# Performance work log

Measured on AMD Instinct MI355X. Metric: run time of the kernel, lower is better.

Reference implementation:

```python
import jax, jax.numpy as jnp
import numpy as np

ALPHA = 0.2  # LeakyReLU negative slope
NEG_INF = -9e15


def setup_inputs() -> dict:
    key = jax.random.key(0)
    k1, k2, k3, k4 = jax.random.split(key, 4)
    B, N, F_in, F_out = 8, 2048, 256, 128
    x = jax.random.normal(k1, (B, N, F_in), dtype=jnp.float32)
    adj = jax.random.randint(k2, (B, N, N), 0, 2, dtype=jnp.int32)
    # xavier-uniform-like init
    limW = float(np.sqrt(6.0 / (F_in + F_out)))
    W = jax.random.uniform(k3, (F_in, F_out), jnp.float32, -limW, limW)
    lima = float(np.sqrt(6.0 / (2 * F_out + 1)))
    a = jax.random.uniform(k4, (2 * F_out, 1), jnp.float32, -lima, lima)
    return {"x": x, "adj": adj, "W": W, "a": a}


def reference(x, adj, W, a):
    # x: [B, N, F_in], adj: [B, N, N], W: [F_in, F_out], a: [2*F_out, 1]
    F_out = W.shape[1]
    h = jnp.einsum('bnf,fo->bno', x, W)            # [B, N, F_out]
    a1 = a[:F_out, 0]                               # attends to source node i
    a2 = a[F_out:, 0]                               # attends to target node j
    f1 = h @ a1                                     # [B, N]
    f2 = h @ a2                                     # [B, N]
    # e[b,i,j] = leakyrelu(a1.h_i + a2.h_j) -- factored form of the concat trick
    e = jax.nn.leaky_relu(f1[:, :, None] + f2[:, None, :], negative_slope=ALPHA)
    attention = jnp.where(adj > 0, e, NEG_INF)
    attention = jax.nn.softmax(attention, axis=2)   # [B, N, N]
    # dropout is identity in eval mode
    h_prime = jnp.einsum('bij,bjo->bio', attention, h)  # [B, N, F_out]
    return jax.nn.elu(h_prime)                      # concat=True -> ELU
```

## Files before the change

### kernel.cpp

```cpp
#include <hip/hip_runtime.h>
#include <stdint.h>

#define BB   8
#define NN   2048
#define FIN  256
#define FOUT 128

using short8 = __attribute__((ext_vector_type(8))) short;
using f32x4  = __attribute__((ext_vector_type(4))) float;

__device__ __forceinline__ unsigned short rbf(float f) {
    return (unsigned short)((__float_as_uint(f) + 0x8000u) >> 16);
}

__device__ __forceinline__ void mfma_calib(int m, int quad, int* Mlab, int* Nlab) {
    short8 pa1, pb1, pa2, pb2;
    const short one = (short)0x3F80;
    const short mb  = (short)rbf((float)m);
#pragma unroll
    for (int j = 0; j < 8; ++j) { pa1[j] = 0; pa2[j] = 0; pb1[j] = mb; pb2[j] = one; }
    if (quad == 0) { pa1[0] = one; pa2[0] = mb; }
    f32x4 zz = {0.f, 0.f, 0.f, 0.f};
    f32x4 c1 = __builtin_amdgcn_mfma_f32_16x16x32_bf16(pa1, pb1, zz, 0, 0, 0);
    f32x4 c2 = __builtin_amdgcn_mfma_f32_16x16x32_bf16(pa2, pb2, zz, 0, 0, 0);
#pragma unroll
    for (int r = 0; r < 4; ++r) {
        Nlab[r] = ((int)c1[r]) & 15;
        Mlab[r] = ((int)c2[r]) & 15;
    }
}

__global__ __launch_bounds__(256) void gat_wt(const float* __restrict__ W,
                                              unsigned short* __restrict__ wt) {
    const int g  = blockIdx.x * 256 + threadIdx.x;
    const int k  = g >> 5;
    const int o4 = (g & 31) << 2;
    float4 wv = *(const float4*)(W + (k << 7) + o4);
    wt[((o4 + 0) << 8) + k] = rbf(wv.x);
    wt[((o4 + 1) << 8) + k] = rbf(wv.y);
    wt[((o4 + 2) << 8) + k] = rbf(wv.z);
    wt[((o4 + 3) << 8) + k] = rbf(wv.w);
}

__global__ __launch_bounds__(256) void gat_h3(
        const float* __restrict__ x, const unsigned short* __restrict__ wt,
        const float* __restrict__ a, unsigned short* __restrict__ ht,
        float* __restrict__ f1, float* __restrict__ f2) {
    __shared__ unsigned short xs[16][264];
    __shared__ float hs[16][132];
    const int bk   = blockIdx.x;
    const int R0   = bk << 4;
    const int b    = R0 >> 11;
    const int il0  = R0 & (NN - 1);
    const int tid  = threadIdx.x;
    const int w    = tid >> 6;
    const int lane = tid & 63;
    const int m    = lane & 15;
    const int quad = lane >> 4;

#pragma unroll
    for (int rr = 0; rr < 4; ++rr) {
        const int row = (w << 2) + rr;
        float4 xv = *(const float4*)(x + (size_t)(R0 + row) * FIN + (lane << 2));
        ushort4 c4;
        c4.x = rbf(xv.x); c4.y = rbf(xv.y); c4.z = rbf(xv.z); c4.w = rbf(xv.w);
        *(ushort4*)(&xs[row][lane << 2]) = c4;
    }
    int Mlab[4], Nlab[4];
    mfma_calib(m, quad, Mlab, Nlab);
    __syncthreads();

    f32x4 zz = {0.f, 0.f, 0.f, 0.f};
    f32x4 acc[2] = {zz, zz};
#pragma unroll
    for (int kc = 0; kc < 8; ++kc) {
        const int k0 = (kc << 5) + (quad << 3);
        short8 av = *(const short8*)(&xs[m][k0]);
#pragma unroll
        for (int t = 0; t < 2; ++t) {
            const int ot = (w << 1) + t;
            short8 bw = *(const short8*)(wt + (((ot << 4) + m) << 8) + k0);
            acc[t] = __builtin_amdgcn_mfma_f32_16x16x32_bf16(av, bw, acc[t], 0, 0, 0);
        }
    }
#pragma unroll
    for (int t = 0; t < 2; ++t)
#pragma unroll
        for (int r = 0; r < 4; ++r)
            hs[Mlab[r]][(((w << 1) + t) << 4) + Nlab[r]] = acc[t][r];
    __syncthreads();

    {
        const int i   = tid >> 4;
        const int seg = tid & 15;
        const int o0  = seg << 3;
        float s1 = 0.f, s2 = 0.f;
#pragma unroll
        for (int e = 0; e < 8; ++e) {
            float hv = hs[i][o0 + e];
            s1 = fmaf(hv, a[o0 + e], s1);
            s2 = fmaf(hv, a[FOUT + o0 + e], s2);
        }
        s1 += __shfl_xor(s1, 1); s1 += __shfl_xor(s1, 2);
        s1 += __shfl_xor(s1, 4); s1 += __shfl_xor(s1, 8);
        s2 += __shfl_xor(s2, 1); s2 += __shfl_xor(s2, 2);
        s2 += __shfl_xor(s2, 4); s2 += __shfl_xor(s2, 8);
        if (seg == 0) { f1[R0 + i] = s1; f2[R0 + i] = s2; }
    }
    {
        const int o  = tid >> 1;
        const int i8 = (tid & 1) << 3;
        short8 hv;
#pragma unroll
        for (int e = 0; e < 8; ++e) hv[e] = (short)rbf(hs[i8 + e][o]);
        *(short8*)(ht + ((size_t)((b << 7) + o) << 11) + il0 + i8) = hv;
    }
}

__global__ __launch_bounds__(256, 2) void gat_s4(
        const int* __restrict__ adj, const unsigned short* __restrict__ ht,
        const float* __restrict__ f1, const float* __restrict__ f2,
        float* __restrict__ out) {
    const int bk   = blockIdx.x;
    const int b    = bk & 7;
    const int i0   = (bk >> 3) << 5;
    const int tid  = threadIdx.x;
    const int w    = tid >> 6;
    const int lane = tid & 63;
    const int m    = lane & 15;
    const int quad = lane >> 4;

    __shared__ float accb[2][32][128];
    __shared__ float sbuf[4][2][16];

    int Mlab[4], Nlab[4];
    mfma_calib(m, quad, Mlab, Nlab);

    const int gi0 = (b << 11) + i0;
    const float f1a = f1[gi0 + m];
    const float f1b = f1[gi0 + 16 + m];
    const int* adjr0 = adj + ((size_t)(gi0 + m) << 11);
    const int* adjr1 = adj + ((size_t)(gi0 + 16 + m) << 11);
    const float* f2b = f2 + (b << 11);
    const unsigned short* htb = ht + ((size_t)b << 18);

    f32x4 zz = {0.f, 0.f, 0.f, 0.f};
    f32x4 acc1[8], acc2[8];
#pragma unroll
    for (int t = 0; t < 8; ++t) { acc1[t] = zz; acc2[t] = zz; }
    float s1 = 0.f, s2 = 0.f;

    const int jb = (w << 9) + (quad << 3);
#pragma unroll 2
    for (int c = 0; c < 16; ++c) {
        const int j0 = jb + (c << 5);
        short8 hf[8];
#pragma unroll
        for (int ot = 0; ot < 8; ++ot)
            hf[ot] = *(const short8*)(htb + ((size_t)((ot << 4) + m) << 11) + j0);

        int4   aA0 = *(const int4*)(adjr0 + j0);
        int4   aA1 = *(const int4*)(adjr0 + j0 + 4);
        int4   aB0 = *(const int4*)(adjr1 + j0);
        int4   aB1 = *(const int4*)(adjr1 + j0 + 4);
        float4 fa  = *(const float4*)(f2b + j0);
        float4 fb  = *(const float4*)(f2b + j0 + 4);
        float fm[8] = {fa.x, fa.y, fa.z, fa.w, fb.x, fb.y, fb.z, fb.w};

        float pA[8], pB[8];
        {
            int am[8] = {aA0.x, aA0.y, aA0.z, aA0.w, aA1.x, aA1.y, aA1.z, aA1.w};
#pragma unroll
            for (int u = 0; u < 8; ++u) {
                float e = f1a + fm[u];
                pA[u] = (am[u] > 0) ? __expf(fmaxf(e, 0.2f * e)) : 0.f;
            }
        }
        {
            int bm[8] = {aB0.x, aB0.y, aB0.z, aB0.w, aB1.x, aB1.y, aB1.z, aB1.w};
#pragma unroll
            for (int u = 0; u < 8; ++u) {
                float e = f1b + fm[u];
                pB[u] = (bm[u] > 0) ? __expf(fmaxf(e, 0.2f * e)) : 0.f;
            }
        }
        s1 += ((pA[0] + pA[1]) + (pA[2] + pA[3])) + ((pA[4] + pA[5]) + (pA[6] + pA[7]));
        s2 += ((pB[0] + pB[1]) + (pB[2] + pB[3])) + ((pB[4] + pB[5]) + (pB[6] + pB[7]));

        short8 pf1, pf2;
#pragma unroll
        for (int u = 0; u < 8; ++u) { pf1[u] = (short)rbf(pA[u]); pf2[u] = (short)rbf(pB[u]); }

#pragma unroll
        for (int ot = 0; ot < 8; ++ot) {
            acc1[ot] = __builtin_amdgcn_mfma_f32_16x16x32_bf16(pf1, hf[ot], acc1[ot], 0, 0, 0);
            acc2[ot] = __builtin_amdgcn_mfma_f32_16x16x32_bf16(pf2, hf[ot], acc2[ot], 0, 0, 0);
        }
    }

    s1 += __shfl_xor(s1, 16); s1 += __shfl_xor(s1, 32);
    s2 += __shfl_xor(s2, 16); s2 += __shfl_xor(s2, 32);
    if (lane < 16) { sbuf[w][0][lane] = s1; sbuf[w][1][lane] = s2; }

    if (w < 2) {
#pragma unroll
        for (int ot = 0; ot < 8; ++ot)
#pragma unroll
            for (int r = 0; r < 4; ++r) {
                accb[w][Mlab[r]][(ot << 4) + Nlab[r]]      = acc1[ot][r];
                accb[w][16 + Mlab[r]][(ot << 4) + Nlab[r]] = acc2[ot][r];
            }
    }
    __syncthreads();
    if (w >= 2) {
#pragma unroll
        for (int ot = 0; ot < 8; ++ot)
#pragma unroll
            for (int r = 0; r < 4; ++r) {
                accb[w - 2][Mlab[r]][(ot << 4) + Nlab[r]]      += acc1[ot][r];
                accb[w - 2][16 + Mlab[r]][(ot << 4) + Nlab[r]] += acc2[ot][r];
            }
    }
    __syncthreads();

    {
        const int row = tid >> 3;
        const int o0  = (tid & 7) << 4;
        const int g   = row >> 4;
        const int mm  = row & 15;
        const float s = (sbuf[0][g][mm] + sbuf[1][g][mm]) +
                        (sbuf[2][g][mm] + sbuf[3][g][mm]);
        const float inv = 1.0f / s;
        float* orow = out + (((size_t)gi0 + row) << 7) + o0;
#pragma unroll
        for (int v4 = 0; v4 < 4; ++v4) {
            float4 rv;
            float y;
            y = (accb[0][row][o0 + 4 * v4 + 0] + accb[1][row][o0 + 4 * v4 + 0]) * inv;
            rv.x = y > 0.f ? y : expm1f(y);
            y = (accb[0][row][o0 + 4 * v4 + 1] + accb[1][row][o0 + 4 * v4 + 1]) * inv;
            rv.y = y > 0.f ? y : expm1f(y);
            y = (accb[0][row][o0 + 4 * v4 + 2] + accb[1][row][o0 + 4 * v4 + 2]) * inv;
            rv.z = y > 0.f ? y : expm1f(y);
            y = (accb[0][row][o0 + 4 * v4 + 3] + accb[1][row][o0 + 4 * v4 + 3]) * inv;
            rv.w = y > 0.f ? y : expm1f(y);
            *(float4*)(orow + 4 * v4) = rv;
        }
    }
}

extern "C" void kernel_launch(void* const* d_in, const int* in_sizes, int n_in,
                              void* d_out, int out_size, void* d_ws, size_t ws_size,
                              hipStream_t stream) {
    const float* x   = nullptr;
    const int*   adj = nullptr;
    const float* W   = nullptr;
    const float* a   = nullptr;
    for (int i = 0; i < n_in; ++i) {
        const long s = in_sizes[i];
        if      (s == (long)BB * NN * NN)  adj = (const int*)d_in[i];
        else if (s == (long)BB * NN * FIN) x   = (const float*)d_in[i];
        else if (s == (long)FIN * FOUT)    W   = (const float*)d_in[i];
        else if (s == 2L * FOUT)           a   = (const float*)d_in[i];
    }
    if (!x)   x   = (const float*)d_in[0];
    if (!adj) adj = (const int*)d_in[1];
    if (!W)   W   = (const float*)d_in[2];
    if (!a)   a   = (const float*)d_in[3];
    float* out = (float*)d_out;

    unsigned short* wt = (unsigned short*)d_ws;
    unsigned short* ht = wt + 32768;
    float* f1 = (float*)(ht + (size_t)BB * NN * FOUT);
    float* f2 = f1 + BB * NN;

    hipLaunchKernelGGL(gat_wt, dim3(32),   dim3(256), 0, stream, W, wt);
    hipLaunchKernelGGL(gat_h3, dim3(1024), dim3(256), 0, stream, x, wt, a, ht, f1, f2);
    hipLaunchKernelGGL(gat_s4, dim3(512),  dim3(256), 0, stream, adj, ht, f1, f2, out);
}
```

Measured before the change: 247.0 us.

## Process 64 rows per block to reuse h fragments across four row groups

The attention kernel now handles 64 query rows per block instead of 32. Each loaded h^T fragment feeds four row groups of MFMAs rather than two, which halves the global and L2 reads of h per output row. The cross-wave reduction becomes a rotating four-phase accumulate into one padded shared buffer. In exchange the block count halves to 256, below the number of CUs, and launch bounds drop to one block per SM with 128 accumulator registers per lane, which may reduce occupancy and latency hiding on the adj stream.

```diff
diff --git a/kernel.cpp b/kernel.cpp
--- a/kernel.cpp
+++ b/kernel.cpp
@@ -117,41 +117,45 @@
     }
 }
 
-__global__ __launch_bounds__(256, 2) void gat_s4(
+__global__ __launch_bounds__(256, 1) void gat_s5(
         const int* __restrict__ adj, const unsigned short* __restrict__ ht,
         const float* __restrict__ f1, const float* __restrict__ f2,
         float* __restrict__ out) {
     const int bk   = blockIdx.x;
     const int b    = bk & 7;
-    const int i0   = (bk >> 3) << 5;
+    const int i0   = (bk >> 3) << 6;
     const int tid  = threadIdx.x;
     const int w    = tid >> 6;
     const int lane = tid & 63;
     const int m    = lane & 15;
     const int quad = lane >> 4;
 
-    __shared__ float accb[2][32][128];
-    __shared__ float sbuf[4][2][16];
+    __shared__ float accb[64][132];
+    __shared__ float sbuf[4][4][16];
 
     int Mlab[4], Nlab[4];
     mfma_calib(m, quad, Mlab, Nlab);
 
     const int gi0 = (b << 11) + i0;
-    const float f1a = f1[gi0 + m];
-    const float f1b = f1[gi0 + 16 + m];
-    const int* adjr0 = adj + ((size_t)(gi0 + m) << 11);
-    const int* adjr1 = adj + ((size_t)(gi0 + 16 + m) << 11);
+    float f1v[4];
+    const int* adjr[4];
+#pragma unroll
+    for (int g = 0; g < 4; ++g) {
+        f1v[g]  = f1[gi0 + (g << 4) + m];
+        adjr[g] = adj + ((size_t)(gi0 + (g << 4) + m) << 11);
+    }
     const float* f2b = f2 + (b << 11);
     const unsigned short* htb = ht + ((size_t)b << 18);
 
     f32x4 zz = {0.f, 0.f, 0.f, 0.f};
-    f32x4 acc1[8], acc2[8];
-#pragma unroll
-    for (int t = 0; t < 8; ++t) { acc1[t] = zz; acc2[t] = zz; }
-    float s1 = 0.f, s2 = 0.f;
+    f32x4 acc[4][8];
+#pragma unroll
+    for (int g = 0; g < 4; ++g)
+#pragma unroll
+        for (int t = 0; t < 8; ++t) acc[g][t] = zz;
+    float sp[4] = {0.f, 0.f, 0.f, 0.f};
 
     const int jb = (w << 9) + (quad << 3);
-#pragma unroll 2
     for (int c = 0; c < 16; ++c) {
         const int j0 = jb + (c << 5);
         short8 hf[8];
@@ -159,73 +163,61 @@
         for (int ot = 0; ot < 8; ++ot)
             hf[ot] = *(const short8*)(htb + ((size_t)((ot << 4) + m) << 11) + j0);
 
-        int4   aA0 = *(const int4*)(adjr0 + j0);
-        int4   aA1 = *(const int4*)(adjr0 + j0 + 4);
-        int4   aB0 = *(const int4*)(adjr1 + j0);
-        int4   aB1 = *(const int4*)(adjr1 + j0 + 4);
-        float4 fa  = *(const float4*)(f2b + j0);
-        float4 fb  = *(const float4*)(f2b + j0 + 4);
+        float4 fa = *(const float4*)(f2b + j0);
+        float4 fb = *(const float4*)(f2b + j0 + 4);
         float fm[8] = {fa.x, fa.y, fa.z, fa.w, fb.x, fb.y, fb.z, fb.w};
 
-        float pA[8], pB[8];
-        {
-            int am[8] = {aA0.x, aA0.y, aA0.z, aA0.w, aA1.x, aA1.y, aA1.z, aA1.w};
+#pragma unroll
+        for (int g = 0; g < 4; ++g) {
+            int4 a0 = *(const int4*)(adjr[g] + j0);
+            int4 a1 = *(const int4*)(adjr[g] + j0 + 4);
+            int am[8] = {a0.x, a0.y, a0.z, a0.w, a1.x, a1.y, a1.z, a1.w};
+            const float f1r = f1v[g];
+            float p[8];
 #pragma unroll
             for (int u = 0; u < 8; ++u) {
-                float e = f1a + fm[u];
-                pA[u] = (am[u] > 0) ? __expf(fmaxf(e, 0.2f * e)) : 0.f;
+                float e = f1r + fm[u];
+                p[u] = (am[u] > 0) ? __expf(fmaxf(e, 0.2f * e)) : 0.f;
             }
-        }
-        {
-            int bm[8] = {aB0.x, aB0.y, aB0.z, aB0.w, aB1.x, aB1.y, aB1.z, aB1.w};
-#pragma unroll
-            for (int u = 0; u < 8; ++u) {
-                float e = f1b + fm[u];
-                pB[u] = (bm[u] > 0) ? __expf(fmaxf(e, 0.2f * e)) : 0.f;
-            }
-        }
-        s1 += ((pA[0] + pA[1]) + (pA[2] + pA[3])) + ((pA[4] + pA[5]) + (pA[6] + pA[7]));
-        s2 += ((pB[0] + pB[1]) + (pB[2] + pB[3])) + ((pB[4] + pB[5]) + (pB[6] + pB[7]));
-
-        short8 pf1, pf2;
-#pragma unroll
-        for (int u = 0; u < 8; ++u) { pf1[u] = (short)rbf(pA[u]); pf2[u] = (short)rbf(pB[u]); }
-
-#pragma unroll
-        for (int ot = 0; ot < 8; ++ot) {
-            acc1[ot] = __builtin_amdgcn_mfma_f32_16x16x32_bf16(pf1, hf[ot], acc1[ot], 0, 0, 0);
-            acc2[ot] = __builtin_amdgcn_mfma_f32_16x16x32_bf16(pf2, hf[ot], acc2[ot], 0, 0, 0);
-        }
-    }
-
-    s1 += __shfl_xor(s1, 16); s1 += __shfl_xor(s1, 32);
-    s2 += __shfl_xor(s2, 16); s2 += __shfl_xor(s2, 32);
-    if (lane < 16) { sbuf[w][0][lane] = s1; sbuf[w][1][lane] = s2; }
-
-    if (w < 2) {
-#pragma unroll
-        for (int ot = 0; ot < 8; ++ot)
-#pragma unroll
-            for (int r = 0; r < 4; ++r) {
-                accb[w][Mlab[r]][(ot << 4) + Nlab[r]]      = acc1[ot][r];
-                accb[w][16 + Mlab[r]][(ot << 4) + Nlab[r]] = acc2[ot][r];
-            }
-    }
-    __syncthreads();
-    if (w >= 2) {
-#pragma unroll
-        for (int ot = 0; ot < 8; ++ot)
-#pragma unroll
-            for (int r = 0; r < 4; ++r) {
-                accb[w - 2][Mlab[r]][(ot << 4) + Nlab[r]]      += acc1[ot][r];
-                accb[w - 2][16 + Mlab[r]][(ot << 4) + Nlab[r]] += acc2[ot][r];
-            }
-    }
-    __syncthreads();
+            sp[g] += ((p[0] + p[1]) + (p[2] + p[3])) + ((p[4] + p[5]) + (p[6] + p[7]));
+            short8 pf;
+#pragma unroll
+            for (int u = 0; u < 8; ++u) pf[u] = (short)rbf(p[u]);
+#pragma unroll
+            for (int ot = 0; ot < 8; ++ot)
+                acc[g][ot] = __builtin_amdgcn_mfma_f32_16x16x32_bf16(pf, hf[ot], acc[g][ot], 0, 0, 0);
+        }
+    }
+
+#pragma unroll
+    for (int g = 0; g < 4; ++g) {
+        float v = sp[g];
+        v += __shfl_xor(v, 16); v += __shfl_xor(v, 32);
+        if (lane < 16) sbuf[w][g][lane] = v;
+    }
+
+#pragma unroll
+    for (int p = 0; p < 4; ++p) {
+        const int g = (w + p) & 3;
+        if (p == 0) {
+#pragma unroll
+            for (int ot = 0; ot < 8; ++ot)
+#pragma unroll
+                for (int r = 0; r < 4; ++r)
+                    accb[(g << 4) + Mlab[r]][(ot << 4) + Nlab[r]] = acc[g][ot][r];
+        } else {
+#pragma unroll
+            for (int ot = 0; ot < 8; ++ot)
+#pragma unroll
+                for (int r = 0; r < 4; ++r)
+                    accb[(g << 4) + Mlab[r]][(ot << 4) + Nlab[r]] += acc[g][ot][r];
+        }
+        __syncthreads();
+    }
 
     {
-        const int row = tid >> 3;
-        const int o0  = (tid & 7) << 4;
+        const int row = tid >> 2;
+        const int o0  = (tid & 3) << 5;
         const int g   = row >> 4;
         const int mm  = row & 15;
         const float s = (sbuf[0][g][mm] + sbuf[1][g][mm]) +
@@ -233,17 +225,13 @@
         const float inv = 1.0f / s;
         float* orow = out + (((size_t)gi0 + row) << 7) + o0;
 #pragma unroll
-        for (int v4 = 0; v4 < 4; ++v4) {
+        for (int v4 = 0; v4 < 8; ++v4) {
             float4 rv;
             float y;
-            y = (accb[0][row][o0 + 4 * v4 + 0] + accb[1][row][o0 + 4 * v4 + 0]) * inv;
-            rv.x = y > 0.f ? y : expm1f(y);
-            y = (accb[0][row][o0 + 4 * v4 + 1] + accb[1][row][o0 + 4 * v4 + 1]) * inv;
-            rv.y = y > 0.f ? y : expm1f(y);
-            y = (accb[0][row][o0 + 4 * v4 + 2] + accb[1][row][o0 + 4 * v4 + 2]) * inv;
-            rv.z = y > 0.f ? y : expm1f(y);
-            y = (accb[0][row][o0 + 4 * v4 + 3] + accb[1][row][o0 + 4 * v4 + 3]) * inv;
-            rv.w = y > 0.f ? y : expm1f(y);
+            y = accb[row][o0 + 4 * v4 + 0] * inv; rv.x = y > 0.f ? y : expm1f(y);
+            y = accb[row][o0 + 4 * v4 + 1] * inv; rv.y = y > 0.f ? y : expm1f(y);
+            y = accb[row][o0 + 4 * v4 + 2] * inv; rv.z = y > 0.f ? y : expm1f(y);
+            y = accb[row][o0 + 4 * v4 + 3] * inv; rv.w = y > 0.f ? y : expm1f(y);
             *(float4*)(orow + 4 * v4) = rv;
         }
     }
@@ -276,5 +264,5 @@
 
     hipLaunchKernelGGL(gat_wt, dim3(32),   dim3(256), 0, stream, W, wt);
     hipLaunchKernelGGL(gat_h3, dim3(1024), dim3(256), 0, stream, x, wt, a, ht, f1, f2);
-    hipLaunchKernelGGL(gat_s4, dim3(512),  dim3(256), 0, stream, adj, ht, f1, f2, out);
-}
+    hipLaunchKernelGGL(gat_s5, dim3(256),  dim3(256), 0, stream, adj, ht, f1, f2, out);
+}
```

Result: slower. 274.6 us (+11.2%).
